# Kernel tuning notes

Measured on AMD Instinct MI355X. Metric: run time of the kernel, lower is better.

## Reference

```python
import jax, jax.numpy as jnp
import numpy as np

NUM_HEADS = 16
NUM_FEATURES = 256
EPSILON = 1e-4


def _gaussian_orthogonal_matrix(num_rows, num_cols, seed=0):
    # Stacked transposed-Q blocks from QR of Gaussian blocks, scaled by sqrt(num_cols)
    rng = np.random.default_rng(seed)
    blocks = []
    for _ in range(num_rows // num_cols):
        a = rng.standard_normal((num_cols, num_cols))
        qm, _ = np.linalg.qr(a)
        blocks.append(qm.T)
    rem = num_rows - (num_rows // num_cols) * num_cols
    if rem > 0:
        a = rng.standard_normal((num_cols, num_cols))
        qm, _ = np.linalg.qr(a)
        blocks.append(qm.T[:rem])
    mat = np.concatenate(blocks, axis=0) * np.sqrt(num_cols)
    return jnp.asarray(mat, dtype=jnp.float32)


def setup_inputs() -> dict:
    key = jax.random.key(0)
    kq, kk, kv = jax.random.split(key, 3)
    B, L, D = 4, 4096, 1024
    q = jax.random.normal(kq, (B, L, D), dtype=jnp.float32)
    k = jax.random.normal(kk, (B, L, D), dtype=jnp.float32)
    v = jax.random.normal(kv, (B, L, D), dtype=jnp.float32)
    W = _gaussian_orthogonal_matrix(NUM_FEATURES, D // NUM_HEADS)
    return {"q": q, "k": k, "v": v, "W": W}


def _split_heads(x, H):
    B, L, D = x.shape
    return x.reshape(B, L, H, D // H).transpose(0, 2, 1, 3)  # [B,H,L,d]


def _phi(x, W, is_query, eps):
    # x: [B,H,L,d], W: [m,d]
    h = -0.5 * jnp.sum(x * x, axis=-1, keepdims=True)          # [B,H,L,1]
    proj = jnp.einsum('bhld,md->bhlm', x, W)                   # [B,H,L,m]
    # For queries, max over last dim of h (size-1) == h itself; for keys, global max.
    stab = h if is_query else jnp.max(h)
    ker = jnp.exp(h + proj - stab)
    m = W.shape[0]
    return (m ** -0.5) * (ker + eps)


def reference(q, k, v, W):
    H = NUM_HEADS
    eps = EPSILON
    B, L, D = q.shape
    scale = D ** -0.25  # note: uses full model dim, as in the original code
    qh = _split_heads(q, H) * scale
    kh = _split_heads(k, H) * scale
    vh = _split_heads(v, H)
    q_prime = _phi(qh, W, True, eps)   # [B,H,L,m]
    k_prime = _phi(kh, W, False, eps)  # [B,H,L,m]
    # denominator: q' @ sum_l k'
    d_ = jnp.einsum('bhlm,bhm->bhl', q_prime, jnp.sum(k_prime, axis=-2))[..., None]
    d_ = d_ + 2.0 * eps * (jnp.abs(d_) <= eps).astype(d_.dtype)
    kv = jnp.einsum('bhlm,bhld->bhmd', k_prime, vh)            # [B,H,m,d]
    out = jnp.einsum('bhlm,bhmd->bhld', q_prime, kv) / d_      # [B,H,L,d]
    return out.transpose(0, 2, 1, 3).reshape(B, L, D)
```

## Files before the change

### kernel.cpp

```cpp
#include <hip/hip_runtime.h>


typedef unsigned short u16;
typedef __attribute__((ext_vector_type(8))) short s8v;
typedef __attribute__((ext_vector_type(4))) float f4v;

#define NB 4
#define NL 4096
#define ND 1024
#define NH 16
#define HDIM 64
#define NM 256

#define SCALE 0.17677669529663687f
#define RSQM 0.0625f
#define FEPS 1e-4f
#define ECLAMP 80.0f

#define MFMA16(a, b, c) __builtin_amdgcn_mfma_f32_16x16x32_bf16((a), (b), (c), 0, 0, 0)

__device__ __forceinline__ u16 f2bf(float x) {
  unsigned u = __float_as_uint(x);
  u += 0x7FFFu + ((u >> 16) & 1u);
  return (u16)(u >> 16);
}
__device__ __forceinline__ float bf2f(u16 b) {
  return __uint_as_float(((unsigned)b) << 16);
}
__device__ __forceinline__ u16 bhi(float x) {
  return (u16)(__float_as_uint(x) >> 16);
}
__device__ __forceinline__ float bhif(float x) {
  return __uint_as_float(__float_as_uint(x) & 0xFFFF0000u);
}

__device__ __forceinline__ void mk2t(const float4& a, const float4& b, float sc,
                                     s8v& hi, s8v& lo, float& ss) {
  float f[8] = {a.x * sc, a.y * sc, a.z * sc, a.w * sc,
                b.x * sc, b.y * sc, b.z * sc, b.w * sc};
#pragma unroll
  for (int e = 0; e < 8; e++) {
    ss = fmaf(f[e], f[e], ss);
    hi[e] = (short)bhi(f[e]);
    lo[e] = (short)bhi(f[e] - bhif(f[e]));
  }
}

__global__ void prep_kernel(const float* __restrict__ wp, u16* __restrict__ WfH,
                            u16* __restrict__ WfL, float* __restrict__ kvx) {
  const int idx = blockIdx.x * 512 + threadIdx.x;
  const int e = idx & 7, ln = (idx >> 3) & 63, mt = (idx >> 9) & 15, kk = idx >> 13;
  const int m = mt * 16 + (ln & 15);
  const int d = kk * 32 + ((ln >> 4) << 3) + e;
  const float x = wp[m * HDIM + d];
  const u16 hh = f2bf(x);
  WfH[idx] = hh;
  WfL[idx] = f2bf(x - bf2f(hh));
  for (int i = idx; i < 64 * 256 * 80; i += 16384) kvx[i] = 0.f;
}

__global__ __launch_bounds__(512, 4) void kv_kernel(
    const float* __restrict__ kg, const float* __restrict__ vg,
    const u16* __restrict__ WfH, const u16* __restrict__ WfL,
    float* __restrict__ kvx) {
  const int bh = blockIdx.x >> 3, ch = blockIdx.x & 7;
  const int b = bh >> 4, h = bh & 15;
  const int tid = threadIdx.x, lane = tid & 63, w = tid >> 6;
  const int l15 = lane & 15, g = lane >> 4;

  __shared__ __align__(16) u16 kpH[256][40];
  __shared__ __align__(16) u16 kpL[256][40];
  __shared__ __align__(16) u16 VfH[4][64][8];
  __shared__ __align__(16) u16 VfL[4][64][8];

  const int rt = w & 1, mg = w >> 1;
  const int mtb = 2 * w;
  const int vct = w & 3, vhl = w >> 2;

  f4v zero4 = {0.f, 0.f, 0.f, 0.f};
  f4v acc[2][5];
#pragma unroll
  for (int i = 0; i < 2; i++)
#pragma unroll
    for (int j = 0; j < 5; j++) acc[i][j] = zero4;

  s8v oneh = {0, 0, 0, 0, 0, 0, 0, 0};
  if (l15 == 0) {
#pragma unroll
    for (int e = 0; e < 8; e++) oneh[e] = (short)0x3F80;
  }

  for (int it = 0; it < 16; it++) {
    const int rbase = ch * 512 + it * 32;
    const float* vb =
        vg + (size_t)(b * NL + rbase + 8 * g) * ND + h * HDIM + vct * 16 + l15;
    float vx[8];
#pragma unroll
    for (int e = 0; e < 8; e++) vx[e] = vb[(size_t)e * ND];
    const float* kb = kg + (size_t)(b * NL + rbase + rt * 16 + l15) * ND + h * HDIM;
    const float4 ka0 = *(const float4*)(kb + g * 8);
    const float4 ka1 = *(const float4*)(kb + g * 8 + 4);
    const float4 ka2 = *(const float4*)(kb + 32 + g * 8);
    const float4 ka3 = *(const float4*)(kb + 32 + g * 8 + 4);
    s8v a0h, a0l, a1h, a1l;
    float ss = 0.f;
    mk2t(ka0, ka1, SCALE, a0h, a0l, ss);
    mk2t(ka2, ka3, SCALE, a1h, a1l, ss);
    ss += __shfl_xor(ss, 16);
    ss += __shfl_xor(ss, 32);
    const float cneg = -0.5f * ss;
    float ccr[4];
#pragma unroll
    for (int r = 0; r < 4; r++) ccr[r] = __shfl(cneg, 4 * g + r);

    s8v vf;
    if (vhl == 0) {
#pragma unroll
      for (int e = 0; e < 8; e++) vf[e] = (short)bhi(vx[e]);
    } else {
#pragma unroll
      for (int e = 0; e < 8; e++) vf[e] = (short)bhi(vx[e] - bhif(vx[e]));
    }

    int itz = it;
    asm volatile("" : "+v"(itz));
    const u16* WfHp = WfH + (itz & 0x7FFF0000);
    const u16* WfLp = WfL + (itz & 0x7FFF0000);

    u16 hs[4][4], ls[4][4];
#pragma unroll
    for (int mi = 0; mi < 4; mi++) {
      const int mt = mg * 4 + mi;
      const s8v b0h = *(const s8v*)(WfHp + (size_t)(mt * 64 + lane) * 8);
      const s8v b0l = *(const s8v*)(WfLp + (size_t)(mt * 64 + lane) * 8);
      const s8v b1h = *(const s8v*)(WfHp + (size_t)((16 + mt) * 64 + lane) * 8);
      const s8v b1l = *(const s8v*)(WfLp + (size_t)((16 + mt) * 64 + lane) * 8);
      f4v p = zero4;
      p = MFMA16(a0h, b0h, p);
      p = MFMA16(a1h, b1h, p);
      p = MFMA16(a0h, b0l, p);
      p = MFMA16(a1h, b1l, p);
      p = MFMA16(a0l, b0h, p);
      p = MFMA16(a1l, b1h, p);
#pragma unroll
      for (int r = 0; r < 4; r++) {
        const float arg = fminf(p[r] + ccr[r], ECLAMP);
        const float kv_ = RSQM * __expf(arg) + (RSQM * FEPS);
        hs[mi][r] = bhi(kv_);
        ls[mi][r] = bhi(kv_ - bhif(kv_));
      }
    }
    __syncthreads();
#pragma unroll
    for (int mi = 0; mi < 4; mi++) {
      const int m = (mg * 4 + mi) * 16 + l15;
      *(ushort4*)&kpH[m][rt * 16 + 4 * g] =
          make_ushort4(hs[mi][0], hs[mi][1], hs[mi][2], hs[mi][3]);
      *(ushort4*)&kpL[m][rt * 16 + 4 * g] =
          make_ushort4(ls[mi][0], ls[mi][1], ls[mi][2], ls[mi][3]);
    }
    {
      u16(*vdst)[64][8] = vhl ? VfL : VfH;
      *(s8v*)&vdst[vct][lane][0] = vf;
    }
    __syncthreads();

    const s8v A0h = *(const s8v*)&kpH[mtb * 16 + l15][8 * g];
    const s8v A0l = *(const s8v*)&kpL[mtb * 16 + l15][8 * g];
    const s8v A1h = *(const s8v*)&kpH[(mtb + 1) * 16 + l15][8 * g];
    const s8v A1l = *(const s8v*)&kpL[(mtb + 1) * 16 + l15][8 * g];
#pragma unroll
    for (int ct = 0; ct < 4; ct++) {
      const s8v vh = *(const s8v*)&VfH[ct][lane][0];
      const s8v vl = *(const s8v*)&VfL[ct][lane][0];
      acc[0][ct] = MFMA16(A0h, vh, acc[0][ct]);
      acc[0][ct] = MFMA16(A0h, vl, acc[0][ct]);
      acc[0][ct] = MFMA16(A0l, vh, acc[0][ct]);
      acc[1][ct] = MFMA16(A1h, vh, acc[1][ct]);
      acc[1][ct] = MFMA16(A1h, vl, acc[1][ct]);
      acc[1][ct] = MFMA16(A1l, vh, acc[1][ct]);
    }
    acc[0][4] = MFMA16(A0h, oneh, acc[0][4]);
    acc[0][4] = MFMA16(A0l, oneh, acc[0][4]);
    acc[1][4] = MFMA16(A1h, oneh, acc[1][4]);
    acc[1][4] = MFMA16(A1l, oneh, acc[1][4]);
  }

  float* kvb = kvx + (size_t)bh * (256 * 80);
#pragma unroll
  for (int mi = 0; mi < 2; mi++)
#pragma unroll
    for (int ct = 0; ct < 5; ct++)
#pragma unroll
      for (int r = 0; r < 4; r++) {
        const int m = (mtb + mi) * 16 + 4 * g + r;
        const int c = ct * 16 + l15;
        atomicAdd(&kvb[m * 80 + c], acc[mi][ct][r]);
      }
}

__global__ __launch_bounds__(512) void fragk_kernel(const float* __restrict__ kvx,
                                                    u16* __restrict__ kvfH,
                                                    u16* __restrict__ kvfL) {
  const int bh = blockIdx.x;
  const float* kb = kvx + (size_t)bh * (256 * 80);
  for (int f = threadIdx.x; f < 20480; f += 512) {
    const int kk = f / 2560;
    const int r1 = f - kk * 2560;
    const int ct = r1 >> 9;
    const int r2 = r1 & 511;
    const int ln = r2 >> 3, e = r2 & 7;
    const int m = kk * 32 + ((ln >> 4) << 3) + e;
    const int c = ct * 16 + (ln & 15);
    const float x = kb[m * 80 + c];
    const u16 hh = f2bf(x);
    kvfH[(size_t)bh * 20480 + f] = hh;
    kvfL[(size_t)bh * 20480 + f] = f2bf(x - bf2f(hh));
  }
}

__global__ __launch_bounds__(512, 4) void out_kernel(
    const float* __restrict__ qg, const u16* __restrict__ WfH,
    const u16* __restrict__ WfL, const u16* __restrict__ kvfH,
    const u16* __restrict__ kvfL, float* __restrict__ outp) {
  const int bh = blockIdx.x >> 6, lt = blockIdx.x & 63;
  const int b = bh >> 4, h = bh & 15;
  const int tid = threadIdx.x, lane = tid & 63, w = tid >> 6;
  const int l15 = lane & 15, g = lane >> 4;

  __shared__ __align__(16) u16 qpH[64][264];
  __shared__ __align__(16) u16 qpL[64][264];
  __shared__ float dinv[64];

  const int rt = w & 3, mh = w >> 2;

  {
    const float* qb = qg + (size_t)(b * NL + lt * 64 + rt * 16 + l15) * ND + h * HDIM;
    const float4 qa0 = *(const float4*)(qb + g * 8);
    const float4 qa1 = *(const float4*)(qb + g * 8 + 4);
    const float4 qa2 = *(const float4*)(qb + 32 + g * 8);
    const float4 qa3 = *(const float4*)(qb + 32 + g * 8 + 4);
    s8v a0h, a0l, a1h, a1l;
    float ss = 0.f;
    mk2t(qa0, qa1, SCALE, a0h, a0l, ss);
    mk2t(qa2, qa3, SCALE, a1h, a1l, ss);
    f4v zero4 = {0.f, 0.f, 0.f, 0.f};
#pragma unroll
    for (int mi = 0; mi < 8; mi++) {
      const int mt = mh * 8 + mi;
      const s8v b0h = *(const s8v*)(WfH + (size_t)(mt * 64 + lane) * 8);
      const s8v b0l = *(const s8v*)(WfL + (size_t)(mt * 64 + lane) * 8);
      const s8v b1h = *(const s8v*)(WfH + (size_t)((16 + mt) * 64 + lane) * 8);
      const s8v b1l = *(const s8v*)(WfL + (size_t)((16 + mt) * 64 + lane) * 8);
      f4v p = zero4;
      p = MFMA16(a0h, b0h, p);
      p = MFMA16(a1h, b1h, p);
      p = MFMA16(a0h, b0l, p);
      p = MFMA16(a1h, b1l, p);
      p = MFMA16(a0l, b0h, p);
      p = MFMA16(a1l, b1h, p);
#pragma unroll
      for (int r = 0; r < 4; r++) {
        const float arg = fminf(p[r], ECLAMP);
        const float qv = RSQM * __expf(arg) + (RSQM * FEPS);
        qpH[rt * 16 + 4 * g + r][mt * 16 + l15] = bhi(qv);
        qpL[rt * 16 + 4 * g + r][mt * 16 + l15] = bhi(qv - bhif(qv));
      }
    }
  }
  __syncthreads();

  const int ctA = (w < 4) ? 0 : 2;
  const int ctB = ctA + 1;
  f4v o0 = {0.f, 0.f, 0.f, 0.f}, o1 = o0, o2 = o0;
  const size_t fb = (size_t)bh * (8 * 5 * 512);
#pragma unroll
  for (int kk = 0; kk < 8; kk++) {
    const s8v A2h = *(const s8v*)&qpH[rt * 16 + l15][kk * 32 + 8 * g];
    const s8v A2l = *(const s8v*)&qpL[rt * 16 + l15][kk * 32 + 8 * g];
    const size_t bA = fb + (size_t)((kk * 5 + ctA) * 64 + lane) * 8;
    const s8v BAh = *(const s8v*)(kvfH + bA);
    const s8v BAl = *(const s8v*)(kvfL + bA);
    o0 = MFMA16(A2h, BAh, o0);
    o0 = MFMA16(A2h, BAl, o0);
    o0 = MFMA16(A2l, BAh, o0);
    const size_t bB = fb + (size_t)((kk * 5 + ctB) * 64 + lane) * 8;
    const s8v BBh = *(const s8v*)(kvfH + bB);
    const s8v BBl = *(const s8v*)(kvfL + bB);
    o1 = MFMA16(A2h, BBh, o1);
    o1 = MFMA16(A2h, BBl, o1);
    o1 = MFMA16(A2l, BBh, o1);
    if (w < 4) {
      const size_t bC = fb + (size_t)((kk * 5 + 4) * 64 + lane) * 8;
      const s8v BCh = *(const s8v*)(kvfH + bC);
      const s8v BCl = *(const s8v*)(kvfL + bC);
      o2 = MFMA16(A2h, BCh, o2);
      o2 = MFMA16(A2h, BCl, o2);
      o2 = MFMA16(A2l, BCh, o2);
    }
  }
  if (w < 4 && l15 == 0) {
#pragma unroll
    for (int r = 0; r < 4; r++) {
      float d = o2[r];
      if (fabsf(d) <= FEPS) d += 2.0f * FEPS;
      dinv[rt * 16 + 4 * g + r] = 1.0f / d;
    }
  }
  __syncthreads();
  {
    float* ob = outp + (size_t)(b * NL + lt * 64) * ND + h * HDIM;
#pragma unroll
    for (int r = 0; r < 4; r++) {
      const int row = rt * 16 + 4 * g + r;
      const float di = dinv[row];
      ob[(size_t)row * ND + ctA * 16 + l15] = o0[r] * di;
      ob[(size_t)row * ND + ctB * 16 + l15] = o1[r] * di;
    }
  }
}

extern "C" void kernel_launch(void* const* d_in, const int* in_sizes, int n_in,
                              void* d_out, int out_size, void* d_ws, size_t ws_size,
                              hipStream_t stream) {
  const float* q = (const float*)d_in[0];
  const float* k = (const float*)d_in[1];
  const float* v = (const float*)d_in[2];
  const float* w = (const float*)d_in[3];
  float* out = (float*)d_out;

  u16* WfH = (u16*)d_ws;
  u16* WfL = WfH + 16384;
  float* kvx = (float*)((char*)d_ws + 65536);
  u16* kvfH = (u16*)((char*)d_ws + 65536 + (size_t)64 * 256 * 80 * 4);
  u16* kvfL = kvfH + (size_t)64 * 20480;

  prep_kernel<<<32, 512, 0, stream>>>(w, WfH, WfL, kvx);
  kv_kernel<<<512, 512, 0, stream>>>(k, v, WfH, WfL, kvx);
  fragk_kernel<<<64, 512, 0, stream>>>(kvx, kvfH, kvfL);
  out_kernel<<<4096, 512, 0, stream>>>(q, WfH, WfL, kvfH, kvfL, out);
}
```

Baseline: 399.0 us.

## Split kv and output kernels across more blocks and compute denominator via k-sum dot

The kv kernel now splits the 256 features into two halves across blocks, doubling the grid and halving per-thread accumulators and shared memory. The out kernel processes 32 rows per block instead of 64, and computes the denominator as a scalar dot product of q' with a separately extracted k-sum vector instead of an extra MFMA column tile. The aim is more parallelism and occupancy and less MFMA work, at the cost of recomputing k features twice per row chunk (once per feature half) and loading W fragments more often.

```diff
diff --git a/kernel.cpp b/kernel.cpp
--- a/kernel.cpp
+++ b/kernel.cpp
@@ -5,10 +5,8 @@
 typedef __attribute__((ext_vector_type(8))) short s8v;
 typedef __attribute__((ext_vector_type(4))) float f4v;
 
-#define NB 4
 #define NL 4096
 #define ND 1024
-#define NH 16
 #define HDIM 64
 #define NM 256
 
@@ -45,44 +43,54 @@
     lo[e] = (short)bhi(f[e] - bhif(f[e]));
   }
 }
+__device__ __forceinline__ void mk2q(const float4& a, const float4& b, float sc,
+                                     s8v& hi, s8v& lo) {
+  float f[8] = {a.x * sc, a.y * sc, a.z * sc, a.w * sc,
+                b.x * sc, b.y * sc, b.z * sc, b.w * sc};
+#pragma unroll
+  for (int e = 0; e < 8; e++) {
+    hi[e] = (short)bhi(f[e]);
+    lo[e] = (short)bhi(f[e] - bhif(f[e]));
+  }
+}
 
 __global__ void prep_kernel(const float* __restrict__ wp, u16* __restrict__ WfH,
                             u16* __restrict__ WfL, float* __restrict__ kvx) {
   const int idx = blockIdx.x * 512 + threadIdx.x;
-  const int e = idx & 7, ln = (idx >> 3) & 63, mt = (idx >> 9) & 15, kk = idx >> 13;
-  const int m = mt * 16 + (ln & 15);
-  const int d = kk * 32 + ((ln >> 4) << 3) + e;
-  const float x = wp[m * HDIM + d];
-  const u16 hh = f2bf(x);
-  WfH[idx] = hh;
-  WfL[idx] = f2bf(x - bf2f(hh));
-  for (int i = idx; i < 64 * 256 * 80; i += 16384) kvx[i] = 0.f;
-}
-
-__global__ __launch_bounds__(512, 4) void kv_kernel(
+  if (idx < 16384) {
+    const int e = idx & 7, ln = (idx >> 3) & 63, mt = (idx >> 9) & 15, kk = idx >> 13;
+    const int m = mt * 16 + (ln & 15);
+    const int d = kk * 32 + ((ln >> 4) << 3) + e;
+    const float x = wp[m * HDIM + d];
+    const u16 hh = f2bf(x);
+    WfH[idx] = hh;
+    WfL[idx] = f2bf(x - bf2f(hh));
+  }
+  for (int i = idx; i < 64 * 256 * 80; i += 65536) kvx[i] = 0.f;
+}
+
+__global__ __launch_bounds__(512, 8) void kv_kernel(
     const float* __restrict__ kg, const float* __restrict__ vg,
     const u16* __restrict__ WfH, const u16* __restrict__ WfL,
     float* __restrict__ kvx) {
-  const int bh = blockIdx.x >> 3, ch = blockIdx.x & 7;
+  const int bx = blockIdx.x;
+  const int mh = bx >> 9, bh = (bx >> 3) & 63, ch = bx & 7;
   const int b = bh >> 4, h = bh & 15;
   const int tid = threadIdx.x, lane = tid & 63, w = tid >> 6;
   const int l15 = lane & 15, g = lane >> 4;
 
-  __shared__ __align__(16) u16 kpH[256][40];
-  __shared__ __align__(16) u16 kpL[256][40];
+  __shared__ __align__(16) u16 kpH[128][40];
+  __shared__ __align__(16) u16 kpL[128][40];
   __shared__ __align__(16) u16 VfH[4][64][8];
   __shared__ __align__(16) u16 VfL[4][64][8];
 
   const int rt = w & 1, mg = w >> 1;
-  const int mtb = 2 * w;
   const int vct = w & 3, vhl = w >> 2;
 
   f4v zero4 = {0.f, 0.f, 0.f, 0.f};
-  f4v acc[2][5];
-#pragma unroll
-  for (int i = 0; i < 2; i++)
-#pragma unroll
-    for (int j = 0; j < 5; j++) acc[i][j] = zero4;
+  f4v acc[5];
+#pragma unroll
+  for (int j = 0; j < 5; j++) acc[j] = zero4;
 
   s8v oneh = {0, 0, 0, 0, 0, 0, 0, 0};
   if (l15 == 0) {
@@ -127,10 +135,10 @@
     const u16* WfHp = WfH + (itz & 0x7FFF0000);
     const u16* WfLp = WfL + (itz & 0x7FFF0000);
 
-    u16 hs[4][4], ls[4][4];
-#pragma unroll
-    for (int mi = 0; mi < 4; mi++) {
-      const int mt = mg * 4 + mi;
+    u16 hs[2][4], ls[2][4];
+#pragma unroll
+    for (int mi = 0; mi < 2; mi++) {
+      const int mt = mh * 8 + mg * 2 + mi;
       const s8v b0h = *(const s8v*)(WfHp + (size_t)(mt * 64 + lane) * 8);
       const s8v b0l = *(const s8v*)(WfLp + (size_t)(mt * 64 + lane) * 8);
       const s8v b1h = *(const s8v*)(WfHp + (size_t)((16 + mt) * 64 + lane) * 8);
@@ -152,11 +160,11 @@
     }
     __syncthreads();
 #pragma unroll
-    for (int mi = 0; mi < 4; mi++) {
-      const int m = (mg * 4 + mi) * 16 + l15;
-      *(ushort4*)&kpH[m][rt * 16 + 4 * g] =
+    for (int mi = 0; mi < 2; mi++) {
+      const int ml = (mg * 2 + mi) * 16 + l15;
+      *(ushort4*)&kpH[ml][rt * 16 + 4 * g] =
           make_ushort4(hs[mi][0], hs[mi][1], hs[mi][2], hs[mi][3]);
-      *(ushort4*)&kpL[m][rt * 16 + 4 * g] =
+      *(ushort4*)&kpL[ml][rt * 16 + 4 * g] =
           make_ushort4(ls[mi][0], ls[mi][1], ls[mi][2], ls[mi][3]);
     }
     {
@@ -165,89 +173,84 @@
     }
     __syncthreads();
 
-    const s8v A0h = *(const s8v*)&kpH[mtb * 16 + l15][8 * g];
-    const s8v A0l = *(const s8v*)&kpL[mtb * 16 + l15][8 * g];
-    const s8v A1h = *(const s8v*)&kpH[(mtb + 1) * 16 + l15][8 * g];
-    const s8v A1l = *(const s8v*)&kpL[(mtb + 1) * 16 + l15][8 * g];
+    const s8v A0h = *(const s8v*)&kpH[w * 16 + l15][8 * g];
+    const s8v A0l = *(const s8v*)&kpL[w * 16 + l15][8 * g];
 #pragma unroll
     for (int ct = 0; ct < 4; ct++) {
       const s8v vh = *(const s8v*)&VfH[ct][lane][0];
       const s8v vl = *(const s8v*)&VfL[ct][lane][0];
-      acc[0][ct] = MFMA16(A0h, vh, acc[0][ct]);
-      acc[0][ct] = MFMA16(A0h, vl, acc[0][ct]);
-      acc[0][ct] = MFMA16(A0l, vh, acc[0][ct]);
-      acc[1][ct] = MFMA16(A1h, vh, acc[1][ct]);
-      acc[1][ct] = MFMA16(A1h, vl, acc[1][ct]);
-      acc[1][ct] = MFMA16(A1l, vh, acc[1][ct]);
-    }
-    acc[0][4] = MFMA16(A0h, oneh, acc[0][4]);
-    acc[0][4] = MFMA16(A0l, oneh, acc[0][4]);
-    acc[1][4] = MFMA16(A1h, oneh, acc[1][4]);
-    acc[1][4] = MFMA16(A1l, oneh, acc[1][4]);
+      acc[ct] = MFMA16(A0h, vh, acc[ct]);
+      acc[ct] = MFMA16(A0h, vl, acc[ct]);
+      acc[ct] = MFMA16(A0l, vh, acc[ct]);
+    }
+    acc[4] = MFMA16(A0h, oneh, acc[4]);
+    acc[4] = MFMA16(A0l, oneh, acc[4]);
   }
 
   float* kvb = kvx + (size_t)bh * (256 * 80);
 #pragma unroll
-  for (int mi = 0; mi < 2; mi++)
-#pragma unroll
-    for (int ct = 0; ct < 5; ct++)
-#pragma unroll
-      for (int r = 0; r < 4; r++) {
-        const int m = (mtb + mi) * 16 + 4 * g + r;
-        const int c = ct * 16 + l15;
-        atomicAdd(&kvb[m * 80 + c], acc[mi][ct][r]);
-      }
+  for (int ct = 0; ct < 5; ct++)
+#pragma unroll
+    for (int r = 0; r < 4; r++) {
+      if (ct == 4 && l15 != 0) continue;
+      const int m = mh * 128 + w * 16 + 4 * g + r;
+      const int c = ct * 16 + l15;
+      atomicAdd(&kvb[m * 80 + c], acc[ct][r]);
+    }
 }
 
 __global__ __launch_bounds__(512) void fragk_kernel(const float* __restrict__ kvx,
                                                     u16* __restrict__ kvfH,
-                                                    u16* __restrict__ kvfL) {
-  const int bh = blockIdx.x;
+                                                    u16* __restrict__ kvfL,
+                                                    float* __restrict__ ksg) {
+  const int bh = blockIdx.x >> 2, qq = blockIdx.x & 3;
   const float* kb = kvx + (size_t)bh * (256 * 80);
-  for (int f = threadIdx.x; f < 20480; f += 512) {
-    const int kk = f / 2560;
-    const int r1 = f - kk * 2560;
-    const int ct = r1 >> 9;
-    const int r2 = r1 & 511;
+  for (int f = qq * 4096 + threadIdx.x; f < (qq + 1) * 4096; f += 512) {
+    const int kk = f >> 11, ct = (f >> 9) & 3, r2 = f & 511;
     const int ln = r2 >> 3, e = r2 & 7;
     const int m = kk * 32 + ((ln >> 4) << 3) + e;
     const int c = ct * 16 + (ln & 15);
     const float x = kb[m * 80 + c];
     const u16 hh = f2bf(x);
-    kvfH[(size_t)bh * 20480 + f] = hh;
-    kvfL[(size_t)bh * 20480 + f] = f2bf(x - bf2f(hh));
-  }
-}
-
-__global__ __launch_bounds__(512, 4) void out_kernel(
+    kvfH[(size_t)bh * 16384 + f] = hh;
+    kvfL[(size_t)bh * 16384 + f] = f2bf(x - bf2f(hh));
+  }
+  if (qq == 0 && threadIdx.x < 256)
+    ksg[(size_t)bh * 256 + threadIdx.x] = kb[threadIdx.x * 80 + 64];
+}
+
+__global__ __launch_bounds__(512, 8) void out_kernel(
     const float* __restrict__ qg, const u16* __restrict__ WfH,
     const u16* __restrict__ WfL, const u16* __restrict__ kvfH,
-    const u16* __restrict__ kvfL, float* __restrict__ outp) {
-  const int bh = blockIdx.x >> 6, lt = blockIdx.x & 63;
+    const u16* __restrict__ kvfL, const float* __restrict__ ksg,
+    float* __restrict__ outp) {
+  const int bh = blockIdx.x >> 7, lt = blockIdx.x & 127;
   const int b = bh >> 4, h = bh & 15;
   const int tid = threadIdx.x, lane = tid & 63, w = tid >> 6;
   const int l15 = lane & 15, g = lane >> 4;
 
-  __shared__ __align__(16) u16 qpH[64][264];
-  __shared__ __align__(16) u16 qpL[64][264];
-  __shared__ float dinv[64];
-
-  const int rt = w & 3, mh = w >> 2;
+  __shared__ __align__(16) u16 qpH[32][264];
+  __shared__ __align__(16) u16 qpL[32][264];
+  __shared__ float ksl[256];
+  __shared__ float dinv[32];
+
+  const int rt = w & 1, mhg = w >> 1;
+
+  if (tid < 256) ksl[tid] = ksg[(size_t)bh * 256 + tid];
 
   {
-    const float* qb = qg + (size_t)(b * NL + lt * 64 + rt * 16 + l15) * ND + h * HDIM;
+    const float* qb = qg + (size_t)(b * NL + lt * 32 + rt * 16 + l15) * ND + h * HDIM;
     const float4 qa0 = *(const float4*)(qb + g * 8);
     const float4 qa1 = *(const float4*)(qb + g * 8 + 4);
     const float4 qa2 = *(const float4*)(qb + 32 + g * 8);
     const float4 qa3 = *(const float4*)(qb + 32 + g * 8 + 4);
     s8v a0h, a0l, a1h, a1l;
-    float ss = 0.f;
-    mk2t(qa0, qa1, SCALE, a0h, a0l, ss);
-    mk2t(qa2, qa3, SCALE, a1h, a1l, ss);
+    mk2q(qa0, qa1, SCALE, a0h, a0l);
+    mk2q(qa2, qa3, SCALE, a1h, a1l);
     f4v zero4 = {0.f, 0.f, 0.f, 0.f};
 #pragma unroll
-    for (int mi = 0; mi < 8; mi++) {
-      const int mt = mh * 8 + mi;
+    for (int mi = 0; mi < 4; mi++) {
+      const int mt = mhg * 4 + mi;
       const s8v b0h = *(const s8v*)(WfH + (size_t)(mt * 64 + lane) * 8);
       const s8v b0l = *(const s8v*)(WfL + (size_t)(mt * 64 + lane) * 8);
       const s8v b1h = *(const s8v*)(WfH + (size_t)((16 + mt) * 64 + lane) * 8);
@@ -270,52 +273,52 @@
   }
   __syncthreads();
 
-  const int ctA = (w < 4) ? 0 : 2;
-  const int ctB = ctA + 1;
-  f4v o0 = {0.f, 0.f, 0.f, 0.f}, o1 = o0, o2 = o0;
-  const size_t fb = (size_t)bh * (8 * 5 * 512);
+  {
+    const int row = 4 * w + g;
+    const s8v qh0 = *(const s8v*)&qpH[row][l15 * 16];
+    const s8v qh1 = *(const s8v*)&qpH[row][l15 * 16 + 8];
+    const s8v ql0 = *(const s8v*)&qpL[row][l15 * 16];
+    const s8v ql1 = *(const s8v*)&qpL[row][l15 * 16 + 8];
+    float dsum = 0.f;
+#pragma unroll
+    for (int i = 0; i < 8; i++) {
+      const float q0 = bf2f((u16)qh0[i]) + bf2f((u16)ql0[i]);
+      const float q1 = bf2f((u16)qh1[i]) + bf2f((u16)ql1[i]);
+      dsum = fmaf(q0, ksl[l15 * 16 + i], dsum);
+      dsum = fmaf(q1, ksl[l15 * 16 + 8 + i], dsum);
+    }
+    dsum += __shfl_xor(dsum, 1);
+    dsum += __shfl_xor(dsum, 2);
+    dsum += __shfl_xor(dsum, 4);
+    dsum += __shfl_xor(dsum, 8);
+    if (l15 == 0) {
+      float d = dsum;
+      if (fabsf(d) <= FEPS) d += 2.0f * FEPS;
+      dinv[row] = 1.0f / d;
+    }
+  }
+
+  const int rt2 = w >> 2, ctile = w & 3;
+  f4v o0 = {0.f, 0.f, 0.f, 0.f};
+  const size_t fb = (size_t)bh * 16384;
 #pragma unroll
   for (int kk = 0; kk < 8; kk++) {
-    const s8v A2h = *(const s8v*)&qpH[rt * 16 + l15][kk * 32 + 8 * g];
-    const s8v A2l = *(const s8v*)&qpL[rt * 16 + l15][kk * 32 + 8 * g];
-    const size_t bA = fb + (size_t)((kk * 5 + ctA) * 64 + lane) * 8;
+    const s8v A2h = *(const s8v*)&qpH[rt2 * 16 + l15][kk * 32 + 8 * g];
+    const s8v A2l = *(const s8v*)&qpL[rt2 * 16 + l15][kk * 32 + 8 * g];
+    const size_t bA = fb + (size_t)((kk * 4 + ctile) * 64 + lane) * 8;
     const s8v BAh = *(const s8v*)(kvfH + bA);
     const s8v BAl = *(const s8v*)(kvfL + bA);
     o0 = MFMA16(A2h, BAh, o0);
     o0 = MFMA16(A2h, BAl, o0);
     o0 = MFMA16(A2l, BAh, o0);
-    const size_t bB = fb + (size_t)((kk * 5 + ctB) * 64 + lane) * 8;
-    const s8v BBh = *(const s8v*)(kvfH + bB);
-    const s8v BBl = *(const s8v*)(kvfL + bB);
-    o1 = MFMA16(A2h, BBh, o1);
-    o1 = MFMA16(A2h, BBl, o1);
-    o1 = MFMA16(A2l, BBh, o1);
-    if (w < 4) {
-      const size_t bC = fb + (size_t)((kk * 5 + 4) * 64 + lane) * 8;
-      const s8v BCh = *(const s8v*)(kvfH + bC);
-      const s8v BCl = *(const s8v*)(kvfL + bC);
-      o2 = MFMA16(A2h, BCh, o2);
-      o2 = MFMA16(A2h, BCl, o2);
-      o2 = MFMA16(A2l, BCh, o2);
-    }
-  }
-  if (w < 4 && l15 == 0) {
-#pragma unroll
-    for (int r = 0; r < 4; r++) {
-      float d = o2[r];
-      if (fabsf(d) <= FEPS) d += 2.0f * FEPS;
-      dinv[rt * 16 + 4 * g + r] = 1.0f / d;
-    }
   }
   __syncthreads();
   {
-    float* ob = outp + (size_t)(b * NL + lt * 64) * ND + h * HDIM;
+    float* ob = outp + (size_t)(b * NL + lt * 32) * ND + h * HDIM;
 #pragma unroll
     for (int r = 0; r < 4; r++) {
-      const int row = rt * 16 + 4 * g + r;
-      const float di = dinv[row];
-      ob[(size_t)row * ND + ctA * 16 + l15] = o0[r] * di;
-      ob[(size_t)row * ND + ctB * 16 + l15] = o1[r] * di;
+      const int row = rt2 * 16 + 4 * g + r;
+      ob[(size_t)row * ND + ctile * 16 + l15] = o0[r] * dinv[row];
     }
   }
 }
@@ -333,10 +336,11 @@
   u16* WfL = WfH + 16384;
   float* kvx = (float*)((char*)d_ws + 65536);
   u16* kvfH = (u16*)((char*)d_ws + 65536 + (size_t)64 * 256 * 80 * 4);
-  u16* kvfL = kvfH + (size_t)64 * 20480;
-
-  prep_kernel<<<32, 512, 0, stream>>>(w, WfH, WfL, kvx);
-  kv_kernel<<<512, 512, 0, stream>>>(k, v, WfH, WfL, kvx);
-  fragk_kernel<<<64, 512, 0, stream>>>(kvx, kvfH, kvfL);
-  out_kernel<<<4096, 512, 0, stream>>>(q, WfH, WfL, kvfH, kvfL, out);
-}
+  u16* kvfL = kvfH + (size_t)64 * 16384;
+  float* ksg = (float*)((char*)kvfL + (size_t)64 * 16384 * 2);
+
+  prep_kernel<<<128, 512, 0, stream>>>(w, WfH, WfL, kvx);
+  kv_kernel<<<1024, 512, 0, stream>>>(k, v, WfH, WfL, kvx);
+  fragk_kernel<<<256, 512, 0, stream>>>(kvx, kvfH, kvfL, ksg);
+  out_kernel<<<8192, 512, 0, stream>>>(q, WfH, WfL, kvfH, kvfL, ksg, out);
+}
```

After: 601.9 us. +50.9%, slower.
